# Performance work log

Hardware: AMD Instinct MI355X
Metric: run time of the kernel (lower is better)

## Reference

```python
import jax, jax.numpy as jnp
import numpy as np

N_NODES = 50000
N_EDGES = 1_600_000
IN_DIM = 256
OUT_DIM = 128
NEG_SLOPE = 0.01  # F.leaky_relu default


def setup_inputs() -> dict:
    key = jax.random.key(0)
    k1, k2, k3, k4, k5 = jax.random.split(key, 5)
    x = jax.random.normal(k1, (N_NODES, IN_DIM), dtype=jnp.float32)
    # glorot_init: uniform in [-r, r], r = sqrt(6/(in+out))
    r = np.sqrt(6.0 / (IN_DIM + OUT_DIM)).astype(np.float32)
    weight = jax.random.uniform(k2, (IN_DIM, OUT_DIM), dtype=jnp.float32, minval=-r, maxval=r)
    adj_rows = jax.random.randint(k3, (N_EDGES,), 0, N_NODES, dtype=jnp.int64 if jax.config.jax_enable_x64 else jnp.int32)
    adj_cols = jax.random.randint(k4, (N_EDGES,), 0, N_NODES, dtype=jnp.int64 if jax.config.jax_enable_x64 else jnp.int32)
    adj_vals = jax.random.uniform(k5, (N_EDGES,), dtype=jnp.float32)
    return {"x": x, "weight": weight, "adj_vals": adj_vals,
            "adj_rows": adj_rows, "adj_cols": adj_cols}


def reference(x, weight, adj_vals, adj_rows, adj_cols):
    # h = X @ W : [N, OUT_DIM]
    h = x @ weight
    # sparse adj @ h via edge-list SpMM: out[r] += v * h[c]
    msgs = adj_vals[:, None] * h[adj_cols]            # [E, OUT_DIM]
    agg = jax.ops.segment_sum(msgs, adj_rows, num_segments=N_NODES)
    # leaky_relu epilogue
    return jnp.where(agg >= 0, agg, NEG_SLOPE * agg)
```

## Files before the change

kernel.cpp:

```cpp
#include <hip/hip_runtime.h>
#include <hip/hip_fp16.h>

#define N_NODES 50000
#define N_EDGES 1600000
#define IN_DIM 256
#define OUT_DIM 128
#define NEG_SLOPE 0.01f

#define SB_SH     10
#define SB_ROWS   1024
#define NSB       ((N_NODES + SB_ROWS - 1) / SB_ROWS)
#define SEG       208

#define BIN_SH    5
#define BIN_ROWS  32
#define NBIN      ((N_NODES + BIN_ROWS - 1) / BIN_ROWS)
#define NBIN_PAD  (NSB * 32)
#define NPART     8
#define CAPB_TOT  (NPART * SEG)
#define OVF_CAP   65536

#define SCAT_BLOCKS 256
#define CONVW_BLOCKS 8
#define EPB_S (N_EDGES / SCAT_BLOCKS)
#define SCAT_ITERS ((EPB_S + 511) / 512)

typedef _Float16 f16x8 __attribute__((ext_vector_type(8)));
typedef float    f32x4 __attribute__((ext_vector_type(4)));
typedef float    f32x8 __attribute__((ext_vector_type(8)));

__device__ __forceinline__ float lrelu(float v) {
    return v >= 0.f ? v : NEG_SLOPE * v;
}

#define BM 128
#define GEMM_BLOCKS ((N_NODES + BM - 1) / BM)

#define CVT16(lo, hi) do { \
    lo[0]=(_Float16)xr[0].x; lo[1]=(_Float16)xr[0].y; lo[2]=(_Float16)xr[0].z; lo[3]=(_Float16)xr[0].w; \
    lo[4]=(_Float16)xr[1].x; lo[5]=(_Float16)xr[1].y; lo[6]=(_Float16)xr[1].z; lo[7]=(_Float16)xr[1].w; \
    hi[0]=(_Float16)xr[2].x; hi[1]=(_Float16)xr[2].y; hi[2]=(_Float16)xr[2].z; hi[3]=(_Float16)xr[2].w; \
    hi[4]=(_Float16)xr[3].x; hi[5]=(_Float16)xr[3].y; hi[6]=(_Float16)xr[3].z; hi[7]=(_Float16)xr[3].w; \
} while (0)

__global__ __launch_bounds__(256, 2) void gemm_xw_mfma(const float* __restrict__ x,
                                                       const __half* __restrict__ wtl,
                                                       __half* __restrict__ h) {
    __shared__ f16x8 wt8[32 * 128];
    __shared__ f16x8 xs8[2][4][BM];

    const int t    = threadIdx.x;
    const int lane = t & 63;
    const int wv   = t >> 6;
    const int row0 = blockIdx.x * BM;

    {
        const int4* src = (const int4*)wtl;
        int4* dst = (int4*)wt8;
#pragma unroll
        for (int i = 0; i < 16; ++i) dst[i * 256 + t] = src[i * 256 + t];
    }

    const int srow = t >> 1;
    const int skh  = t & 1;
    const int grow = row0 + srow;
    const bool rv  = grow < N_NODES;
    const float* xp = x + (size_t)(rv ? grow : 0) * IN_DIM + skh * 16;

    float4 xr[4];
#pragma unroll
    for (int i = 0; i < 4; ++i)
        xr[i] = rv ? ((const float4*)xp)[i] : make_float4(0.f, 0.f, 0.f, 0.f);
    {
        f16x8 lo, hi;
        CVT16(lo, hi);
        xs8[0][skh * 2 + 0][srow] = lo;
        xs8[0][skh * 2 + 1][srow] = hi;
    }
    __syncthreads();

    f32x4 acc[2][8];
#pragma unroll
    for (int mf = 0; mf < 2; ++mf)
#pragma unroll
        for (int nf = 0; nf < 8; ++nf) acc[mf][nf] = (f32x4){0.f, 0.f, 0.f, 0.f};

    const int kg  = lane >> 4;
    const int l15 = lane & 15;
    const int mb  = (wv << 5) + l15;

#pragma unroll
    for (int ks = 0; ks < 8; ++ks) {
        const int cur = ks & 1;
        if (ks < 7) {
#pragma unroll
            for (int i = 0; i < 4; ++i)
                xr[i] = rv ? ((const float4*)(xp + (ks + 1) * 32))[i]
                           : make_float4(0.f, 0.f, 0.f, 0.f);
        }
        const f16x8 b0 = xs8[cur][kg][mb];
        const f16x8 b1 = xs8[cur][kg][mb + 16];
#pragma unroll
        for (int nf = 0; nf < 8; ++nf) {
            const f16x8 a = wt8[(((ks << 2) | kg) << 7) + (nf << 4) + l15];
            acc[0][nf] = __builtin_amdgcn_mfma_f32_16x16x32_f16(a, b0, acc[0][nf], 0, 0, 0);
            acc[1][nf] = __builtin_amdgcn_mfma_f32_16x16x32_f16(a, b1, acc[1][nf], 0, 0, 0);
        }
        if (ks < 7) {
            f16x8 lo, hi;
            CVT16(lo, hi);
            xs8[cur ^ 1][skh * 2 + 0][srow] = lo;
            xs8[cur ^ 1][skh * 2 + 1][srow] = hi;
            __syncthreads();
        }
    }

    const int rg = lane >> 4;
#pragma unroll
    for (int mf = 0; mf < 2; ++mf) {
        const int m = row0 + (wv << 5) + (mf << 4) + l15;
        if (m < N_NODES) {
            __half* hp = h + (size_t)m * OUT_DIM + (rg << 2);
#pragma unroll
            for (int nf = 0; nf < 8; ++nf) {
                union { ushort4 u; __half f[4]; } o;
                o.f[0] = __float2half(acc[mf][nf][0]);
                o.f[1] = __float2half(acc[mf][nf][1]);
                o.f[2] = __float2half(acc[mf][nf][2]);
                o.f[3] = __float2half(acc[mf][nf][3]);
                *(ushort4*)(hp + (nf << 4)) = o.u;
            }
        }
    }
}

__global__ __launch_bounds__(512) void scatter_coarse(const int* __restrict__ rows,
                                                      const int* __restrict__ cols,
                                                      const float* __restrict__ vals,
                                                      int* __restrict__ ccnt,
                                                      int* __restrict__ ovfcnt,
                                                      int2* __restrict__ cbuf,
                                                      int2* __restrict__ ovfbuf,
                                                      const float* __restrict__ w,
                                                      __half* __restrict__ wtl) {
    if (blockIdx.x >= SCAT_BLOCKS) {
        const int e0 = ((blockIdx.x - SCAT_BLOCKS) * 512 + threadIdx.x) * 8;
        const int k  = e0 >> 7;
        const int n0 = e0 & 127;
        const float4 a = *(const float4*)(w + e0);
        const float4 b = *(const float4*)(w + e0 + 4);
        __half* dst = wtl + ((size_t)((k >> 3) * 128 + n0)) * 8 + (k & 7);
        dst[0]  = __float2half(a.x);
        dst[8]  = __float2half(a.y);
        dst[16] = __float2half(a.z);
        dst[24] = __float2half(a.w);
        dst[32] = __float2half(b.x);
        dst[40] = __float2half(b.y);
        dst[48] = __float2half(b.z);
        dst[56] = __float2half(b.w);
        return;
    }

    __shared__ int lcur[NSB];
    const int t = threadIdx.x;
    const int blk = blockIdx.x;
    const int ebase = blk * EPB_S;

    if (t < NSB) lcur[t] = 0;
    __syncthreads();

#pragma unroll
    for (int k = 0; k < SCAT_ITERS; ++k) {
        const int i = k * 512 + t;
        if (i < EPB_S) {
            const int e = ebase + i;
            const int r = rows[e];
            const int sb = r >> SB_SH;
            const int off = atomicAdd(&lcur[sb], 1);
            const int key = (int)(((unsigned)r << 16) | (unsigned)cols[e]);
            const int vb  = __float_as_int(vals[e]);
            if (off < SEG) {
                cbuf[((size_t)sb * SCAT_BLOCKS + blk) * SEG + off] = make_int2(key, vb);
            } else {
                const int p = atomicAdd(ovfcnt, 1);
                if (p < OVF_CAP) ovfbuf[p] = make_int2(key, vb);
            }
        }
    }
    __syncthreads();

    if (t < NSB) ccnt[t * SCAT_BLOCKS + blk] = min(lcur[t], SEG);
}

__global__ __launch_bounds__(512) void scatter_fine(const int* __restrict__ ccnt,
                                                    int* __restrict__ fcnt,
                                                    int* __restrict__ ovfcnt,
                                                    const int2* __restrict__ cbuf,
                                                    int2* __restrict__ ebuf,
                                                    int2* __restrict__ ovfbuf) {
    __shared__ int lcur[32];
    __shared__ int scnt[32];
    const int t    = threadIdx.x;
    const int sb   = blockIdx.x / NPART;
    const int p    = blockIdx.x % NPART;
    const int wv   = t >> 6;
    const int lane = t & 63;

    if (t < 32) {
        lcur[t] = 0;
        scnt[t] = ccnt[sb * SCAT_BLOCKS + p * 32 + t];
    }
    __syncthreads();

    for (int j = 0; j < 4; ++j) {
        const int seg = (wv << 2) + j;
        const int cnt = scnt[seg];
        const size_t sbase = ((size_t)sb * SCAT_BLOCKS + p * 32 + seg) * SEG;
        for (int i = lane; i < cnt; i += 64) {
            const int2 rc = cbuf[sbase + i];
            const unsigned urow = ((unsigned)rc.x) >> 16;
            const int fb = (int)((urow >> BIN_SH) & 31);
            const int off = atomicAdd(&lcur[fb], 1);
            const int key = (rc.x & 0xFFFF) | (int)((urow & (BIN_ROWS - 1)) << 16);
            if (off < SEG) {
                ebuf[(((size_t)sb * 32 + fb) * NPART + p) * SEG + off] = make_int2(key, rc.y);
            } else {
                const int q = atomicAdd(ovfcnt, 1);
                if (q < OVF_CAP) ovfbuf[q] = rc;
            }
        }
    }
    __syncthreads();

    if (t < 32) fcnt[((sb * 32 + t) * NPART) + p] = min(lcur[t], SEG);
}

#define NCLS 256

#define STAGE(IT, HV, VV) do {                                                  \
    _Pragma("unroll")                                                           \
    for (int q = 0; q < 4; ++q) {                                               \
        const int idx = beg[q] + ((IT) << 2) + grp;                             \
        const bool vld = idx < end[q];                                          \
        const int2 r = srec[vld ? idx : 0];                                     \
        VV[q] = vld ? __int_as_float(r.y) : 0.f;                                \
        HV[q] = *(const f16x8*)(h + (size_t)(r.x & 0xFFFF) * OUT_DIM + (gl << 3)); \
    }                                                                           \
} while (0)

__global__ __launch_bounds__(512, 4) void sort_gather(const int* __restrict__ fcnt,
                                                      const int* __restrict__ ovfcnt,
                                                      const int2* __restrict__ ebuf,
                                                      const int2* __restrict__ ovfbuf,
                                                      const __half* __restrict__ h,
                                                      float* __restrict__ out) {
    __shared__ int2 srec[CAPB_TOT];
    __shared__ int  hist[NCLS];
    __shared__ int  pfx[NCLS];
    __shared__ int  rowoff_l[BIN_ROWS + 1];
    __shared__ int  wsum[4];
    __shared__ int  poff[NPART + 1];

    const int t    = threadIdx.x;
    const int bin  = blockIdx.x;
    const int wv   = t >> 6;
    const int lane = t & 63;

    if (t < NCLS) hist[t] = 0;
    if (t == 0) {
        int a = 0;
        poff[0] = 0;
#pragma unroll
        for (int p = 0; p < NPART; ++p) { a += fcnt[bin * NPART + p]; poff[p + 1] = a; }
    }
    __syncthreads();
    const int cnt = poff[NPART];

#define LOCATE(F, PP, II) do {                                                  \
        PP = 0;                                                                 \
        _Pragma("unroll")                                                       \
        for (int j = 1; j < NPART; ++j) PP += ((F) >= poff[j]);                 \
        II = (F) - poff[PP];                                                    \
    } while (0)

    for (int f = t; f < cnt; f += 512) {
        int p, i; LOCATE(f, p, i);
        const int k = ebuf[((size_t)bin * NPART + p) * SEG + i].x;
        atomicAdd(&hist[(((k >> 16) & 31) << 3) | ((k & 0xFFFF) >> 13)], 1);
    }
    __syncthreads();

    {
        const int v = (t < NCLS) ? hist[t] : 0;
        int s = v;
#pragma unroll
        for (int off = 1; off < 64; off <<= 1) {
            const int u = __shfl_up(s, off);
            if (lane >= off) s += u;
        }
        if (t < NCLS && lane == 63) wsum[wv] = s;
        __syncthreads();
        if (t == 0) {
            int a = 0;
#pragma unroll
            for (int i = 0; i < 4; ++i) { const int c = wsum[i]; wsum[i] = a; a += c; }
        }
        __syncthreads();
        if (t < NCLS) {
            const int incl = s + wsum[wv];
            pfx[t]  = incl;
            hist[t] = incl - v;
        }
    }
    __syncthreads();
    if (t < BIN_ROWS) rowoff_l[t] = t ? pfx[(t << 3) - 1] : 0;
    if (t == BIN_ROWS) rowoff_l[BIN_ROWS] = cnt;
    __syncthreads();

    for (int f = t; f < cnt; f += 512) {
        int p, i; LOCATE(f, p, i);
        const int2 r = ebuf[((size_t)bin * NPART + p) * SEG + i];
        const int cls = (((r.x >> 16) & 31) << 3) | ((r.x & 0xFFFF) >> 13);
        const int pos = atomicAdd(&hist[cls], 1);
        srec[pos] = r;
    }
    __syncthreads();

    const int grp = lane >> 4;
    const int gl  = lane & 15;
    const int r0  = wv << 2;

    int beg[4], end[4];
#pragma unroll
    for (int q = 0; q < 4; ++q) { beg[q] = rowoff_l[r0 + q]; end[q] = rowoff_l[r0 + q + 1]; }
    int nmax = 0;
#pragma unroll
    for (int q = 0; q < 4; ++q) nmax = max(nmax, end[q] - beg[q]);
    const int iters = (nmax + 3) >> 2;

    f32x8 acc[4];
#pragma unroll
    for (int q = 0; q < 4; ++q) acc[q] = (f32x8){0.f,0.f,0.f,0.f,0.f,0.f,0.f,0.f};

    f16x8 hc[4], hn[4];
    float vc[4], vn[4];
    if (iters > 0) STAGE(0, hc, vc);
    for (int it = 0; it < iters; ++it) {
        if (it + 1 < iters) STAGE(it + 1, hn, vn);
#pragma unroll
        for (int q = 0; q < 4; ++q)
#pragma unroll
            for (int j = 0; j < 8; ++j) acc[q][j] += vc[q] * (float)hc[q][j];
#pragma unroll
        for (int q = 0; q < 4; ++q) { hc[q] = hn[q]; vc[q] = vn[q]; }
    }

    int novf = *ovfcnt;
    if (novf > OVF_CAP) novf = OVF_CAP;
    for (int e = 0; e < novf; ++e) {
        const int2 rec = ovfbuf[e];
        const unsigned urow = ((unsigned)rec.x) >> 16;
        if ((int)(urow >> BIN_SH) == bin && grp == 0) {
            const int lr = (int)(urow & (BIN_ROWS - 1)) - r0;
            if (lr >= 0 && lr < 4) {
                const float v = __int_as_float(rec.y);
                const f16x8 hv = *(const f16x8*)(h + (size_t)(rec.x & 0xFFFF) * OUT_DIM + (gl << 3));
#pragma unroll
                for (int q = 0; q < 4; ++q)
                    if (q == lr)
#pragma unroll
                        for (int j = 0; j < 8; ++j) acc[q][j] += v * (float)hv[j];
            }
        }
    }

#pragma unroll
    for (int q = 0; q < 4; ++q)
#pragma unroll
        for (int j = 0; j < 8; ++j) {
            float x = acc[q][j];
            x += __shfl_xor(x, 16);
            x += __shfl_xor(x, 32);
            acc[q][j] = x;
        }

    float res[8];
#pragma unroll
    for (int j = 0; j < 8; ++j) {
        float x = acc[0][j];
        x = (grp == 1) ? acc[1][j] : x;
        x = (grp == 2) ? acc[2][j] : x;
        x = (grp == 3) ? acc[3][j] : x;
        res[j] = lrelu(x);
    }
    const int grow = (bin << BIN_SH) + r0 + grp;
    if (grow < N_NODES) {
        float* op = out + (size_t)grow * OUT_DIM + (gl << 3);
        *(float4*)op       = make_float4(res[0], res[1], res[2], res[3]);
        *(float4*)(op + 4) = make_float4(res[4], res[5], res[6], res[7]);
    }
}

extern "C" void kernel_launch(void* const* d_in, const int* in_sizes, int n_in,
                              void* d_out, int out_size, void* d_ws, size_t ws_size,
                              hipStream_t stream) {
    const float* x    = (const float*)d_in[0];
    const float* w    = (const float*)d_in[1];
    const float* vals = (const float*)d_in[2];
    const int*   rows = (const int*)d_in[3];
    const int*   cols = (const int*)d_in[4];
    float* out = (float*)d_out;

    char* ws = (char*)d_ws;
    size_t off = 0;
    auto alloc = [&](size_t bytes) {
        void* p = ws + off;
        off = (off + bytes + 255) & ~(size_t)255;
        return p;
    };
    int2*  cbuf    = (int2*) alloc((size_t)NSB * SCAT_BLOCKS * SEG * sizeof(int2));
    __half* h      = (__half*)cbuf;
    int2*  ebuf    = (int2*) alloc((size_t)NBIN_PAD * NPART * SEG * sizeof(int2));
    int2*  ovfbuf  = (int2*) alloc((size_t)OVF_CAP * sizeof(int2));
    __half* wtl    = (__half*)alloc((size_t)IN_DIM * OUT_DIM * sizeof(__half));
    int*   ccnt    = (int*)  alloc((size_t)NSB * SCAT_BLOCKS * sizeof(int));
    int*   fcnt    = (int*)  alloc((size_t)NBIN_PAD * NPART * sizeof(int));
    int*   ovfcnt  = (int*)  alloc(sizeof(int));

    hipMemsetAsync(ovfcnt, 0, sizeof(int), stream);

    scatter_coarse<<<SCAT_BLOCKS + CONVW_BLOCKS, 512, 0, stream>>>(rows, cols, vals,
                                                                   ccnt, ovfcnt, cbuf, ovfbuf, w, wtl);
    scatter_fine<<<NSB * NPART, 512, 0, stream>>>(ccnt, fcnt, ovfcnt, cbuf, ebuf, ovfbuf);
    gemm_xw_mfma<<<GEMM_BLOCKS, 256, 0, stream>>>(x, wtl, h);
    sort_gather<<<NBIN, 512, 0, stream>>>(fcnt, ovfcnt, ebuf, ovfbuf, h, out);
}
```

Baseline: 198.2 us.

## Locally sort scatter records in LDS for coalesced writes and stage bin records

Both scatter passes now histogram and prefix-sum their keys in shared memory, sort records into an LDS buffer, and then write contiguous runs to global memory. This replaces scattered atomic-offset writes with coalesced stores. The gather kernel copies its bin records into LDS once, dropping the per-element partition lookup and the second global read, and its prefetch loop becomes branch-free with sched barriers. The cost is more shared memory per block (which may reduce occupancy), extra syncs, and the row being re-encoded for overflow records.

Result: slower. 203.8 us (+2.8%).

```diff
diff --git a/kernel.cpp b/kernel.cpp
--- a/kernel.cpp
+++ b/kernel.cpp
@@ -161,12 +161,40 @@
         return;
     }
 
-    __shared__ int lcur[NSB];
-    const int t = threadIdx.x;
-    const int blk = blockIdx.x;
+    __shared__ int2 lsort[EPB_S];
+    __shared__ int  hist[NSB];
+    __shared__ int  cstart[NSB];
+
+    const int t    = threadIdx.x;
+    const int lane = t & 63;
+    const int blk  = blockIdx.x;
     const int ebase = blk * EPB_S;
 
-    if (t < NSB) lcur[t] = 0;
+    if (t < NSB) hist[t] = 0;
+    __syncthreads();
+
+    int myr[SCAT_ITERS];
+#pragma unroll
+    for (int k = 0; k < SCAT_ITERS; ++k) {
+        const int i = k * 512 + t;
+        myr[k] = -1;
+        if (i < EPB_S) {
+            myr[k] = rows[ebase + i];
+            atomicAdd(&hist[myr[k] >> SB_SH], 1);
+        }
+    }
+    __syncthreads();
+
+    if (t < 64) {
+        const int v = (t < NSB) ? hist[t] : 0;
+        int s = v;
+#pragma unroll
+        for (int off = 1; off < 64; off <<= 1) {
+            const int u = __shfl_up(s, off);
+            if (lane >= off) s += u;
+        }
+        if (t < NSB) { cstart[t] = s - v; hist[t] = s - v; }
+    }
     __syncthreads();
 
 #pragma unroll
@@ -174,22 +202,28 @@
         const int i = k * 512 + t;
         if (i < EPB_S) {
             const int e = ebase + i;
-            const int r = rows[e];
-            const int sb = r >> SB_SH;
-            const int off = atomicAdd(&lcur[sb], 1);
-            const int key = (int)(((unsigned)r << 16) | (unsigned)cols[e]);
-            const int vb  = __float_as_int(vals[e]);
-            if (off < SEG) {
-                cbuf[((size_t)sb * SCAT_BLOCKS + blk) * SEG + off] = make_int2(key, vb);
-            } else {
-                const int p = atomicAdd(ovfcnt, 1);
-                if (p < OVF_CAP) ovfbuf[p] = make_int2(key, vb);
-            }
-        }
-    }
-    __syncthreads();
-
-    if (t < NSB) ccnt[t * SCAT_BLOCKS + blk] = min(lcur[t], SEG);
+            const int r = myr[k];
+            const int pos = atomicAdd(&hist[r >> SB_SH], 1);
+            lsort[pos] = make_int2((int)(((unsigned)r << 16) | (unsigned)cols[e]),
+                                   __float_as_int(vals[e]));
+        }
+    }
+    __syncthreads();
+
+    for (int i = t; i < EPB_S; i += 512) {
+        const int2 rc = lsort[i];
+        const int sb  = (int)(((unsigned)rc.x) >> 16) >> SB_SH;
+        const int off = i - cstart[sb];
+        if (off < SEG) {
+            cbuf[((size_t)sb * SCAT_BLOCKS + blk) * SEG + off] = rc;
+        } else {
+            const int p = atomicAdd(ovfcnt, 1);
+            if (p < OVF_CAP) ovfbuf[p] = rc;
+        }
+    }
+    __syncthreads();
+
+    if (t < NSB) ccnt[t * SCAT_BLOCKS + blk] = min(hist[t] - cstart[t], SEG);
 }
 
 __global__ __launch_bounds__(512) void scatter_fine(const int* __restrict__ ccnt,
@@ -198,17 +232,44 @@
                                                     const int2* __restrict__ cbuf,
                                                     int2* __restrict__ ebuf,
                                                     int2* __restrict__ ovfbuf) {
-    __shared__ int lcur[32];
-    __shared__ int scnt[32];
+    __shared__ int2 lsort[32 * SEG];
+    __shared__ int  hist[32];
+    __shared__ int  cstart[32];
+    __shared__ int  scnt[32];
+    __shared__ int  stot;
+
     const int t    = threadIdx.x;
+    const int lane = t & 63;
+    const int wv   = t >> 6;
     const int sb   = blockIdx.x / NPART;
     const int p    = blockIdx.x % NPART;
-    const int wv   = t >> 6;
-    const int lane = t & 63;
 
     if (t < 32) {
-        lcur[t] = 0;
+        hist[t] = 0;
         scnt[t] = ccnt[sb * SCAT_BLOCKS + p * 32 + t];
+    }
+    __syncthreads();
+
+    for (int j = 0; j < 4; ++j) {
+        const int seg = (wv << 2) + j;
+        const int cnt = scnt[seg];
+        const size_t sbase = ((size_t)sb * SCAT_BLOCKS + p * 32 + seg) * SEG;
+        for (int i = lane; i < cnt; i += 64)
+            atomicAdd(&hist[(cbuf[sbase + i].x >> 21) & 31], 1);
+    }
+    __syncthreads();
+
+    if (t < 32) {
+        const int v = hist[t];
+        int s = v;
+#pragma unroll
+        for (int off = 1; off < 32; off <<= 1) {
+            const int u = __shfl_up(s, off);
+            if (t >= off) s += u;
+        }
+        if (t == 31) stot = s;
+        cstart[t] = s - v;
+        hist[t]   = s - v;
     }
     __syncthreads();
 
@@ -220,19 +281,31 @@
             const int2 rc = cbuf[sbase + i];
             const unsigned urow = ((unsigned)rc.x) >> 16;
             const int fb = (int)((urow >> BIN_SH) & 31);
-            const int off = atomicAdd(&lcur[fb], 1);
-            const int key = (rc.x & 0xFFFF) | (int)((urow & (BIN_ROWS - 1)) << 16);
-            if (off < SEG) {
-                ebuf[(((size_t)sb * 32 + fb) * NPART + p) * SEG + off] = make_int2(key, rc.y);
-            } else {
-                const int q = atomicAdd(ovfcnt, 1);
-                if (q < OVF_CAP) ovfbuf[q] = rc;
+            const int pos = atomicAdd(&hist[fb], 1);
+            lsort[pos] = make_int2((rc.x & 0xFFFF) | (int)((urow & (BIN_ROWS - 1)) << 16)
+                                                   | (fb << 21), rc.y);
+        }
+    }
+    __syncthreads();
+
+    const int tot = stot;
+    for (int i = t; i < tot; i += 512) {
+        const int2 rc = lsort[i];
+        const int fb  = (rc.x >> 21) & 31;
+        const int off = i - cstart[fb];
+        if (off < SEG) {
+            ebuf[(((size_t)sb * 32 + fb) * NPART + p) * SEG + off] = rc;
+        } else {
+            const int q = atomicAdd(ovfcnt, 1);
+            if (q < OVF_CAP) {
+                const int row = (sb << SB_SH) | (fb << BIN_SH) | ((rc.x >> 16) & 31);
+                ovfbuf[q] = make_int2((int)(((unsigned)row << 16) | (unsigned)(rc.x & 0xFFFF)), rc.y);
             }
         }
     }
     __syncthreads();
 
-    if (t < 32) fcnt[((sb * 32 + t) * NPART) + p] = min(lcur[t], SEG);
+    if (t < 32) fcnt[((sb * 32 + t) * NPART) + p] = min(hist[t] - cstart[t], SEG);
 }
 
 #define NCLS 256
@@ -242,7 +315,7 @@
     for (int q = 0; q < 4; ++q) {                                               \
         const int idx = beg[q] + ((IT) << 2) + grp;                             \
         const bool vld = idx < end[q];                                          \
-        const int2 r = srec[vld ? idx : 0];                                     \
+        const int2 r = srec[vld ? idx : last];                                  \
         VV[q] = vld ? __int_as_float(r.y) : 0.f;                                \
         HV[q] = *(const f16x8*)(h + (size_t)(r.x & 0xFFFF) * OUT_DIM + (gl << 3)); \
     }                                                                           \
@@ -254,6 +327,7 @@
                                                       const int2* __restrict__ ovfbuf,
                                                       const __half* __restrict__ h,
                                                       float* __restrict__ out) {
+    __shared__ int2 urec[CAPB_TOT];
     __shared__ int2 srec[CAPB_TOT];
     __shared__ int  hist[NCLS];
     __shared__ int  pfx[NCLS];
@@ -276,17 +350,15 @@
     __syncthreads();
     const int cnt = poff[NPART];
 
-#define LOCATE(F, PP, II) do {                                                  \
-        PP = 0;                                                                 \
-        _Pragma("unroll")                                                       \
-        for (int j = 1; j < NPART; ++j) PP += ((F) >= poff[j]);                 \
-        II = (F) - poff[PP];                                                    \
-    } while (0)
-
-    for (int f = t; f < cnt; f += 512) {
-        int p, i; LOCATE(f, p, i);
-        const int k = ebuf[((size_t)bin * NPART + p) * SEG + i].x;
-        atomicAdd(&hist[(((k >> 16) & 31) << 3) | ((k & 0xFFFF) >> 13)], 1);
+    {
+        const int cp = poff[wv + 1] - poff[wv];
+        const size_t pb = ((size_t)bin * NPART + wv) * SEG;
+        const int ub = poff[wv];
+        for (int i = lane; i < cp; i += 64) {
+            const int2 r = ebuf[pb + i];
+            urec[ub + i] = r;
+            atomicAdd(&hist[(((r.x >> 16) & 31) << 3) | ((r.x & 0xFFFF) >> 13)], 1);
+        }
     }
     __syncthreads();
 
@@ -317,9 +389,8 @@
     if (t == BIN_ROWS) rowoff_l[BIN_ROWS] = cnt;
     __syncthreads();
 
-    for (int f = t; f < cnt; f += 512) {
-        int p, i; LOCATE(f, p, i);
-        const int2 r = ebuf[((size_t)bin * NPART + p) * SEG + i];
+    for (int i = t; i < cnt; i += 512) {
+        const int2 r = urec[i];
         const int cls = (((r.x >> 16) & 31) << 3) | ((r.x & 0xFFFF) >> 13);
         const int pos = atomicAdd(&hist[cls], 1);
         srec[pos] = r;
@@ -329,6 +400,7 @@
     const int grp = lane >> 4;
     const int gl  = lane & 15;
     const int r0  = wv << 2;
+    const int last = cnt > 0 ? cnt - 1 : 0;
 
     int beg[4], end[4];
 #pragma unroll
@@ -342,17 +414,22 @@
 #pragma unroll
     for (int q = 0; q < 4; ++q) acc[q] = (f32x8){0.f,0.f,0.f,0.f,0.f,0.f,0.f,0.f};
 
-    f16x8 hc[4], hn[4];
-    float vc[4], vn[4];
-    if (iters > 0) STAGE(0, hc, vc);
-    for (int it = 0; it < iters; ++it) {
-        if (it + 1 < iters) STAGE(it + 1, hn, vn);
-#pragma unroll
-        for (int q = 0; q < 4; ++q)
-#pragma unroll
-            for (int j = 0; j < 8; ++j) acc[q][j] += vc[q] * (float)hc[q][j];
-#pragma unroll
-        for (int q = 0; q < 4; ++q) { hc[q] = hn[q]; vc[q] = vn[q]; }
+    if (cnt > 0 && iters > 0) {
+        f16x8 hc[4], hn[4];
+        float vc[4], vn[4];
+        STAGE(0, hc, vc);
+        for (int it = 0; it < iters; ++it) {
+            const int itn = (it + 1 < iters) ? it + 1 : it;
+            STAGE(itn, hn, vn);
+            __builtin_amdgcn_sched_barrier(0);
+#pragma unroll
+            for (int q = 0; q < 4; ++q)
+#pragma unroll
+                for (int j = 0; j < 8; ++j) acc[q][j] += vc[q] * (float)hc[q][j];
+            __builtin_amdgcn_sched_barrier(0);
+#pragma unroll
+            for (int q = 0; q < 4; ++q) { hc[q] = hn[q]; vc[q] = vn[q]; }
+        }
     }
 
     int novf = *ovfcnt;
```
